# Kernel optimization log

Measured on AMD Instinct MI355X. Metric: run time of the kernel, lower is better.

The kernel has to match this reference:

```python
import jax, jax.numpy as jnp
import numpy as np

B, SEQ, DIM = 2, 4096, 1024
E, S = 8, 512          # num_slots = seq_len // num_experts
HID = 4 * DIM          # FeedForward hidden: dim * mult
SCALE = DIM ** 0.5     # RMSNorm scale


def rmsnorm(x, gamma):
    # matches F.normalize(x, dim=-1) * dim**0.5 * gamma (eps=1e-12 clamp on the norm)
    n = jnp.linalg.norm(x, axis=-1, keepdims=True)
    return x / jnp.maximum(n, 1e-12) * SCALE * gamma


def setup_inputs() -> dict:
    key = jax.random.key(0)
    ks = jax.random.split(key, 4)
    w_init = lambda k, shape: jax.random.normal(k, shape, dtype=jnp.float32) * 0.02
    return {
        "x": jax.random.normal(ks[0], (B, SEQ, DIM), dtype=jnp.float32),
        "norm_gamma": jnp.ones((DIM,), jnp.float32),
        "slot_norm_gamma": jnp.ones((DIM,), jnp.float32),
        "slot_embeds": jax.random.normal(ks[1], (E, S, DIM), dtype=jnp.float32),
        "w1": w_init(ks[2], (E, DIM, HID)),
        "b1": jnp.zeros((E, HID), jnp.float32),
        "w2": w_init(ks[3], (E, HID, DIM)),
        "b2": jnp.zeros((E, DIM), jnp.float32),
    }


def reference(x, norm_gamma, slot_norm_gamma, slot_embeds, w1, b1, w2, b2):
    xn = rmsnorm(x, norm_gamma)                 # [b, n, d]
    sn = rmsnorm(slot_embeds, slot_norm_gamma)  # [e, s, d]

    logits = jnp.einsum('bnd,esd->bnes', xn, sn)                   # [b, n, e, s]
    dispatch = jax.nn.softmax(logits, axis=1)                      # softmax over tokens n
    b, n, e, s = logits.shape
    combine = jax.nn.softmax(logits.reshape(b, n, e * s), axis=-1) # softmax over (e s)

    slots = jnp.einsum('bnd,bnes->besd', xn, dispatch)             # [b, e, s, d]

    # per-expert FeedForward: Linear -> GELU(exact) -> Linear (dropout=0)
    h = jnp.einsum('besd,edh->besh', slots, w1) + b1[None, :, None, :]
    h = jax.nn.gelu(h, approximate=False)
    eo = jnp.einsum('besh,ehd->besd', h, w2) + b2[None, :, None, :]

    eo = eo.reshape(b, e * s, DIM)                                 # [b, (e s), d]
    out = jnp.einsum('bmd,bnm->bnd', eo, combine)                  # [b, n, d]
    return out
```

## Files before the change

kernel.cpp:

```cpp
#include <hip/hip_runtime.h>
#include <math.h>

#define SEQ    4096
#define DIM    1024
#define NEXP   8
#define NSLOT  512
#define ES     4096
#define HID    4096
#define NB     2
#define RMS_SCALE 32.0f

typedef __attribute__((ext_vector_type(4))) float f32x4;
typedef __attribute__((ext_vector_type(8))) short bf16x8;
typedef __attribute__((ext_vector_type(4))) unsigned short us4;

__device__ __forceinline__ unsigned short f2bf(float f) {
    unsigned u = __float_as_uint(f);
    u += 0x7fff + ((u >> 16) & 1);
    return (unsigned short)(u >> 16);
}
__device__ __forceinline__ float bf2f(unsigned short h) {
    return __uint_as_float(((unsigned)h) << 16);
}
__device__ __forceinline__ float gelu_exact(float x) {
    return 0.5f * x * (1.0f + erff(x * 0.70710678118654752f));
}

#define GLOAD_LDS16(gp, lp) \
    __builtin_amdgcn_global_load_lds((const __attribute__((address_space(1))) void*)(gp), \
                                     (__attribute__((address_space(3))) void*)(lp), 16, 0, 0)

__device__ __forceinline__ unsigned ldsoff(const void* p) {
    return (unsigned)(size_t)(const __attribute__((address_space(3))) void*)p;
}

#define DSR(dst, base, off) asm volatile("ds_read_b128 %0, %1 offset:" off : "=v"(dst) : "v"(base))

template<int ORDER>
__global__ void rmsnorm_split(const float* __restrict__ in, const float* __restrict__ gamma,
                              unsigned short* __restrict__ outc) {
    int row = blockIdx.x;
    int t = threadIdx.x;
    float4 v = reinterpret_cast<const float4*>(in + (size_t)row * DIM)[t];
    float ss = v.x*v.x + v.y*v.y + v.z*v.z + v.w*v.w;
    #pragma unroll
    for (int off = 32; off >= 1; off >>= 1) ss += __shfl_down(ss, off, 64);
    __shared__ float red[4];
    if ((t & 63) == 0) red[t >> 6] = ss;
    __syncthreads();
    float inv = RMS_SCALE / fmaxf(sqrtf(red[0] + red[1] + red[2] + red[3]), 1e-12f);
    float4 g = reinterpret_cast<const float4*>(gamma)[t];
    float f[4] = {v.x*inv*g.x, v.y*inv*g.y, v.z*inv*g.z, v.w*inv*g.w};
    us4 hv, lv;
    #pragma unroll
    for (int q = 0; q < 4; ++q) {
        unsigned short h = f2bf(f[q]);
        hv[q] = h;
        lv[q] = f2bf(f[q] - bf2f(h));
    }
    unsigned short* rb = outc + (size_t)row * 3072;
    *reinterpret_cast<us4*>(&rb[t*4]) = hv;
    if (ORDER == 0) {
        *reinterpret_cast<us4*>(&rb[1024 + t*4]) = hv;
        *reinterpret_cast<us4*>(&rb[2048 + t*4]) = lv;
    } else {
        *reinterpret_cast<us4*>(&rb[1024 + t*4]) = lv;
        *reinterpret_cast<us4*>(&rb[2048 + t*4]) = hv;
    }
}

__global__ void col_stats_partial(const float* __restrict__ logits,
                                  float* __restrict__ pmax, float* __restrict__ psum) {
    int col = blockIdx.x * 256 + threadIdx.x;
    int ch  = blockIdx.y;
    int b   = blockIdx.z;
    const float* base = logits + ((size_t)b * SEQ + (size_t)ch * 512) * ES + col;
    float m = -INFINITY, s = 0.f;
    for (int n = 0; n < 512; ++n) {
        float v = base[(size_t)n * ES];
        float mn = fmaxf(m, v);
        s = s * __expf(m - mn) + __expf(v - mn);
        m = mn;
    }
    size_t idx = ((size_t)b * 8 + ch) * ES + col;
    pmax[idx] = m; psum[idx] = s;
}

__global__ void col_stats_reduce(const float* __restrict__ pmax, const float* __restrict__ psum,
                                 float* __restrict__ cmax, float* __restrict__ cinv) {
    int col = blockIdx.x * 256 + threadIdx.x;
    int b   = blockIdx.y;
    float m = -INFINITY, s = 0.f;
    for (int ch = 0; ch < 8; ++ch) {
        size_t idx = ((size_t)b * 8 + ch) * ES + col;
        float m2 = pmax[idx], s2 = psum[idx];
        float mn = fmaxf(m, m2);
        s = s * __expf(m - mn) + s2 * __expf(m2 - mn);
        m = mn;
    }
    cmax[(size_t)b * ES + col] = m;
    cinv[(size_t)b * ES + col] = 1.0f / s;
}

__global__ void row_stats(const float* __restrict__ logits,
                          float* __restrict__ rmax, float* __restrict__ rinv) {
    int row = blockIdx.x;
    int t = threadIdx.x;
    const float* base = logits + (size_t)row * ES;
    float m = -INFINITY, s = 0.f;
    for (int i = t; i < ES; i += 256) {
        float v = base[i];
        float mn = fmaxf(m, v);
        s = s * __expf(m - mn) + __expf(v - mn);
        m = mn;
    }
    __shared__ float sm[256], ssum[256];
    sm[t] = m; ssum[t] = s;
    __syncthreads();
    for (int off = 128; off >= 1; off >>= 1) {
        if (t < off) {
            float m1 = sm[t], m2 = sm[t+off], s1 = ssum[t], s2 = ssum[t+off];
            float mn = fmaxf(m1, m2);
            sm[t] = mn;
            ssum[t] = s1 * __expf(m1 - mn) + s2 * __expf(m2 - mn);
        }
        __syncthreads();
    }
    if (t == 0) { rmax[row] = sm[0]; rinv[row] = 1.0f / ssum[0]; }
}

__global__ void make_weights(const float* __restrict__ logits,
                             const float* __restrict__ cmax, const float* __restrict__ cinv,
                             const float* __restrict__ rmax, const float* __restrict__ rinv,
                             unsigned short* __restrict__ comb, unsigned short* __restrict__ dispT) {
    int b = blockIdx.z;
    const float* L = logits + (size_t)b * SEQ * ES;
    int n0 = blockIdx.y * 32, e0 = blockIdx.x * 32;
    int t = threadIdx.x;
    int r = t >> 3, c4 = (t & 7) * 4;
    __shared__ unsigned short tile[32][36];
    float4 v = *reinterpret_cast<const float4*>(&L[(size_t)(n0 + r) * ES + e0 + c4]);
    float rm = rmax[b*SEQ + n0 + r], ri = rinv[b*SEQ + n0 + r];
    float vv[4] = {v.x, v.y, v.z, v.w};
    us4 cb;
    #pragma unroll
    for (int q = 0; q < 4; ++q) {
        cb[q] = f2bf(__expf(vv[q] - rm) * ri);
        float dv = __expf(vv[q] - cmax[b*ES + e0 + c4 + q]) * cinv[b*ES + e0 + c4 + q];
        tile[c4 + q][r] = f2bf(dv);
    }
    *reinterpret_cast<us4*>(&comb[(size_t)b*SEQ*ES + (size_t)(n0 + r)*ES + e0 + c4]) = cb;
    __syncthreads();
    us4 o = *reinterpret_cast<us4*>(&tile[t >> 3][(t & 7) * 4]);
    *reinterpret_cast<us4*>(&dispT[(size_t)b*ES*SEQ + (size_t)(e0 + (t >> 3))*SEQ + n0 + (t & 7)*4]) = o;
}

__global__ void transpose_b16(const unsigned short* __restrict__ src, unsigned short* __restrict__ dst,
                              int sld, int dld, long sStride, long dStride) {
    int z = blockIdx.z;
    const unsigned short* S = src + (size_t)z * sStride;
    unsigned short* D = dst + (size_t)z * dStride;
    int r0 = blockIdx.y * 32, c0 = blockIdx.x * 32;
    int t = threadIdx.x;
    __shared__ unsigned short tile[32][36];
    us4 v = *reinterpret_cast<const us4*>(&S[(size_t)(r0 + (t>>3)) * sld + c0 + (t&7)*4]);
    #pragma unroll
    for (int q = 0; q < 4; ++q) tile[(t&7)*4 + q][t>>3] = v[q];
    __syncthreads();
    us4 o = *reinterpret_cast<us4*>(&tile[t >> 3][(t & 7) * 4]);
    *reinterpret_cast<us4*>(&D[(size_t)(c0 + (t>>3)) * dld + r0 + (t&7)*4]) = o;
}

__global__ void transpose_f32_b16(const float* __restrict__ src, unsigned short* __restrict__ dst,
                                  int sld, int dld, long sStride, long dStride) {
    int z = blockIdx.z;
    const float* S = src + (size_t)z * sStride;
    unsigned short* D = dst + (size_t)z * dStride;
    int r0 = blockIdx.y * 32, c0 = blockIdx.x * 32;
    int t = threadIdx.x;
    __shared__ unsigned short tile[32][36];
    float4 v = *reinterpret_cast<const float4*>(&S[(size_t)(r0 + (t>>3)) * sld + c0 + (t&7)*4]);
    float vv[4] = {v.x, v.y, v.z, v.w};
    #pragma unroll
    for (int q = 0; q < 4; ++q) tile[(t&7)*4 + q][t>>3] = f2bf(vv[q]);
    __syncthreads();
    us4 o = *reinterpret_cast<us4*>(&tile[t >> 3][(t & 7) * 4]);
    *reinterpret_cast<us4*>(&D[(size_t)(c0 + (t>>3)) * dld + r0 + (t&7)*4]) = o;
}

template<int EPI, int OM>
__global__ __launch_bounds__(512, 2)
void mfma_gemm256(const unsigned short* __restrict__ A, const unsigned short* __restrict__ B,
                  void* __restrict__ Cv, const float* __restrict__ bias,
                  int N, int K, int lda, int ldb, int ldc,
                  long aStride, long bStride, long cStride, int bMod) {
    __shared__ unsigned short lds[65536];
    const int t = threadIdx.x;
    const int lane = t & 63, wave = t >> 6;
    const int wr = wave >> 2, wc = wave & 3;
    const int z = blockIdx.z, zb = z % bMod;
    const unsigned short* Ab = A + (size_t)z * aStride;
    const unsigned short* Bb = B + (size_t)zb * bStride;
    const int gx = gridDim.x;
    int flat = blockIdx.x + blockIdx.y * gx;
    const int cpx = (gx * gridDim.y) >> 3;
    flat = (flat & 7) * cpx + (flat >> 3);
    const int m0 = (flat / gx) * 256, n0 = (flat % gx) * 256;

    const int sr = t >> 3;
    const int sg = (t & 7) ^ (sr & 7);
    const unsigned short* gA = Ab + (size_t)(m0 + sr) * lda + sg * 8;
    const unsigned short* gB = Bb + (size_t)(n0 + sr) * ldb + sg * 8;
    unsigned short* ldsw = lds + wave * 512;

    const int lr = lane & 15, lk = lane >> 4;
    const unsigned sw0 = (unsigned)(((lk)     ^ (lr & 7)) << 4);
    const unsigned sw1 = (unsigned)(((4 + lk) ^ (lr & 7)) << 4);
    const unsigned l0  = ldsoff(lds);
    const unsigned arow = (unsigned)((wr*128 + lr) * 128);
    const unsigned brow = (unsigned)((wc*64  + lr) * 128);
    const unsigned ab00 = l0 + arow + sw0,          ab10 = l0 + arow + sw1;
    const unsigned bb00 = l0 + 32768 + brow + sw0,  bb10 = l0 + 32768 + brow + sw1;
    const unsigned ab01 = ab00 + 65536, ab11 = ab10 + 65536;
    const unsigned bb01 = bb00 + 65536, bb11 = bb10 + 65536;

    #define STAGE_A(buf, half, tt) do { \
        const unsigned short* _g = gA + (size_t)((half)*128) * lda + (tt)*64; \
        unsigned short* _l = ldsw + (buf)*32768 + (half)*8192; \
        GLOAD_LDS16(_g, _l); \
        GLOAD_LDS16(_g + (size_t)64*lda, _l + 4096); } while(0)
    #define STAGE_B(buf, half, tt) do { \
        const unsigned short* _g = gB + (size_t)((half)*128) * ldb + (tt)*64; \
        unsigned short* _l = ldsw + (buf)*32768 + 16384 + (half)*8192; \
        GLOAD_LDS16(_g, _l); \
        GLOAD_LDS16(_g + (size_t)64*ldb, _l + 4096); } while(0)

    f32x4 acc[8][4] = {};
    bf16x8 a0[4], a1[4], b0[4], b1[4];

    const int NT = K / 64;

    STAGE_B(0, 0, 0); STAGE_B(0, 1, 0);
    STAGE_A(0, 0, 0); STAGE_A(0, 1, 0);
    STAGE_B(1, 0, 1); STAGE_B(1, 1, 1);
    asm volatile("s_waitcnt vmcnt(4)" ::: "memory");
    __builtin_amdgcn_s_barrier();

    #define PHASE_MFMA(MB, NB_) \
        __builtin_amdgcn_s_barrier(); \
        asm volatile("s_waitcnt lgkmcnt(0)" ::: "memory"); \
        __builtin_amdgcn_sched_barrier(0); \
        __builtin_amdgcn_s_setprio(1); \
        _Pragma("unroll") \
        for (int m = 0; m < 4; ++m) { \
            _Pragma("unroll") \
            for (int n = 0; n < 2; ++n) { \
                acc[MB+m][NB_+n] = __builtin_amdgcn_mfma_f32_16x16x32_bf16(a0[m], b0[NB_+n], acc[MB+m][NB_+n], 0, 0, 0); \
                acc[MB+m][NB_+n] = __builtin_amdgcn_mfma_f32_16x16x32_bf16(a1[m], b1[NB_+n], acc[MB+m][NB_+n], 0, 0, 0); \
            } \
        } \
        __builtin_amdgcn_s_setprio(0); \
        __builtin_amdgcn_sched_barrier(0); \
        __builtin_amdgcn_s_barrier();

    for (int tt = 0; tt < NT; tt += 2) {
        const bool pf = (tt + 2 < NT);
        DSR(a0[0], ab00, "0");    DSR(a0[1], ab00, "2048");
        DSR(a0[2], ab00, "4096"); DSR(a0[3], ab00, "6144");
        DSR(a1[0], ab10, "0");    DSR(a1[1], ab10, "2048");
        DSR(a1[2], ab10, "4096"); DSR(a1[3], ab10, "6144");
        DSR(b0[0], bb00, "0");    DSR(b0[1], bb00, "2048");
        DSR(b1[0], bb10, "0");    DSR(b1[1], bb10, "2048");
        STAGE_A(1, 0, tt+1);
        __builtin_amdgcn_sched_barrier(0);
        PHASE_MFMA(0, 0)
        DSR(b0[2], bb00, "4096"); DSR(b0[3], bb00, "6144");
        DSR(b1[2], bb10, "4096"); DSR(b1[3], bb10, "6144");
        STAGE_A(1, 1, tt+1);
        __builtin_amdgcn_sched_barrier(0);
        PHASE_MFMA(0, 2)
        DSR(a0[0], ab00, "8192");  DSR(a0[1], ab00, "10240");
        DSR(a0[2], ab00, "12288"); DSR(a0[3], ab00, "14336");
        DSR(a1[0], ab10, "8192");  DSR(a1[1], ab10, "10240");
        DSR(a1[2], ab10, "12288"); DSR(a1[3], ab10, "14336");
        if (pf) STAGE_B(0, 0, tt+2);
        __builtin_amdgcn_sched_barrier(0);
        PHASE_MFMA(4, 0)
        if (pf) STAGE_B(0, 1, tt+2);
        __builtin_amdgcn_sched_barrier(0);
        __builtin_amdgcn_s_barrier();
        __builtin_amdgcn_sched_barrier(0);
        __builtin_amdgcn_s_setprio(1);
        #pragma unroll
        for (int m = 0; m < 4; ++m) {
            #pragma unroll
            for (int n = 0; n < 2; ++n) {
                acc[4+m][2+n] = __builtin_amdgcn_mfma_f32_16x16x32_bf16(a0[m], b0[2+n], acc[4+m][2+n], 0, 0, 0);
                acc[4+m][2+n] = __builtin_amdgcn_mfma_f32_16x16x32_bf16(a1[m], b1[2+n], acc[4+m][2+n], 0, 0, 0);
            }
        }
        __builtin_amdgcn_s_setprio(0);
        if (pf) { asm volatile("s_waitcnt vmcnt(4)" ::: "memory"); }
        else    { asm volatile("s_waitcnt vmcnt(0)" ::: "memory"); }
        __builtin_amdgcn_sched_barrier(0);
        __builtin_amdgcn_s_barrier();
        DSR(a0[0], ab01, "0");    DSR(a0[1], ab01, "2048");
        DSR(a0[2], ab01, "4096"); DSR(a0[3], ab01, "6144");
        DSR(a1[0], ab11, "0");    DSR(a1[1], ab11, "2048");
        DSR(a1[2], ab11, "4096"); DSR(a1[3], ab11, "6144");
        DSR(b0[0], bb01, "0");    DSR(b0[1], bb01, "2048");
        DSR(b1[0], bb11, "0");    DSR(b1[1], bb11, "2048");
        if (pf) STAGE_A(0, 0, tt+2);
        __builtin_amdgcn_sched_barrier(0);
        PHASE_MFMA(0, 0)
        DSR(b0[2], bb01, "4096"); DSR(b0[3], bb01, "6144");
        DSR(b1[2], bb11, "4096"); DSR(b1[3], bb11, "6144");
        if (pf) STAGE_A(0, 1, tt+2);
        __builtin_amdgcn_sched_barrier(0);
        PHASE_MFMA(0, 2)
        DSR(a0[0], ab01, "8192");  DSR(a0[1], ab01, "10240");
        DSR(a0[2], ab01, "12288"); DSR(a0[3], ab01, "14336");
        DSR(a1[0], ab11, "8192");  DSR(a1[1], ab11, "10240");
        DSR(a1[2], ab11, "12288"); DSR(a1[3], ab11, "14336");
        if (pf) STAGE_B(1, 0, tt+3);
        __builtin_amdgcn_sched_barrier(0);
        PHASE_MFMA(4, 0)
        if (pf) STAGE_B(1, 1, tt+3);
        __builtin_amdgcn_sched_barrier(0);
        __builtin_amdgcn_s_barrier();
        __builtin_amdgcn_sched_barrier(0);
        __builtin_amdgcn_s_setprio(1);
        #pragma unroll
        for (int m = 0; m < 4; ++m) {
            #pragma unroll
            for (int n = 0; n < 2; ++n) {
                acc[4+m][2+n] = __builtin_amdgcn_mfma_f32_16x16x32_bf16(a0[m], b0[2+n], acc[4+m][2+n], 0, 0, 0);
                acc[4+m][2+n] = __builtin_amdgcn_mfma_f32_16x16x32_bf16(a1[m], b1[2+n], acc[4+m][2+n], 0, 0, 0);
            }
        }
        __builtin_amdgcn_s_setprio(0);
        if (pf) { asm volatile("s_waitcnt vmcnt(4)" ::: "memory"); }
        else    { asm volatile("s_waitcnt vmcnt(0)" ::: "memory"); }
        __builtin_amdgcn_sched_barrier(0);
        __builtin_amdgcn_s_barrier();
    }

    const float* bz = (EPI != 0) ? bias + (size_t)zb * N : nullptr;
    long coff = (long)z * cStride;
    int rbase = (lane >> 4) * 4;
    int cbase = lane & 15;
    #pragma unroll
    for (int f = 0; f < 8; ++f) {
        #pragma unroll
        for (int n = 0; n < 4; ++n) {
            int col  = n0 + wc*64 + n*16 + cbase;
            int row0 = m0 + wr*128 + f*16 + rbase;
            float bv = (EPI != 0) ? bz[col] : 0.f;
            float vals[4];
            #pragma unroll
            for (int r = 0; r < 4; ++r) {
                float v = acc[f][n][r] + bv;
                if (EPI == 2) v = gelu_exact(v);
                vals[r] = v;
            }
            if (OM == 0) {
                float* C = (float*)Cv + coff;
                #pragma unroll
                for (int r = 0; r < 4; ++r) C[(size_t)(row0 + r) * ldc + col] = vals[r];
            } else {
                unsigned short* C = (unsigned short*)Cv + coff;
                #pragma unroll
                for (int r = 0; r < 4; ++r) C[(size_t)(row0 + r) * ldc + col] = f2bf(vals[r]);
            }
        }
    }
    #undef STAGE_A
    #undef STAGE_B
    #undef PHASE_MFMA
}

template<int EPI, int OM>
__global__ __launch_bounds__(512, 2)
void mfma_gemmX(const unsigned short* __restrict__ A, const unsigned short* __restrict__ B,
                void* __restrict__ Cv, const float* __restrict__ bias,
                int N, int K, int lda, int ldb, int ldc,
                long aStride, long bStride, long cStride, long cStrideE, int bMod) {
    __shared__ unsigned short lds[49152];
    const int t = threadIdx.x;
    const int lane = t & 63, wave = t >> 6;
    const int wr = wave >> 2, wc = wave & 3;
    const int z = blockIdx.z, zb = z % bMod;
    const unsigned short* Ab = A + (size_t)z * aStride;
    const unsigned short* Bb = B + (size_t)zb * bStride;
    const int gx = gridDim.x;
    int flat = blockIdx.x + blockIdx.y * gx;
    const int cpx = (gx * gridDim.y) >> 3;
    flat = (flat & 7) * cpx + (flat >> 3);
    const int m0 = (flat / gx) * 256, n0 = (flat % gx) * 128;

    const int sr = t >> 3;
    const int sg = (t & 7) ^ (sr & 7);
    const unsigned short* gA = Ab + (size_t)(m0 + sr) * lda + sg * 8;
    const unsigned short* gB = Bb + (size_t)(n0 + sr) * ldb + sg * 8;
    unsigned short* ldsw = lds + wave * 512;

    const int lr = lane & 15, lk = lane >> 4;
    const unsigned g0 = (unsigned)(((lk)     ^ (lr & 7)) << 4);
    const unsigned g1 = (unsigned)(((4 + lk) ^ (lr & 7)) << 4);
    const unsigned l0 = ldsoff(lds);
    const unsigned arow = (unsigned)((wr*128 + lr) * 128);
    const unsigned brow = (unsigned)((wc*32  + lr) * 128);
    const unsigned axk0 = l0 + arow + g0,          axk1 = l0 + arow + g1;
    const unsigned bxk0 = l0 + 32768 + brow + g0,  bxk1 = l0 + 32768 + brow + g1;

    #define STAGE_AX(buf, half, tt) do { \
        const unsigned short* _g = gA + (size_t)((half)*128) * lda + (tt)*64; \
        unsigned short* _l = ldsw + (buf)*24576 + (half)*8192; \
        GLOAD_LDS16(_g, _l); \
        GLOAD_LDS16(_g + (size_t)64*lda, _l + 4096); } while(0)
    #define STAGE_BX(buf, tt) do { \
        const unsigned short* _g = gB + (tt)*64; \
        unsigned short* _l = ldsw + (buf)*24576 + 16384; \
        GLOAD_LDS16(_g, _l); \
        GLOAD_LDS16(_g + (size_t)64*ldb, _l + 4096); } while(0)

    f32x4 acc[8][2] = {};
    bf16x8 a0[4], a1[4], b0[2], b1[2];

    const int NT = K / 64;

    STAGE_BX(0, 0);
    STAGE_AX(0, 0, 0); STAGE_AX(0, 1, 0);
    STAGE_BX(1, 1);
    asm volatile("s_waitcnt vmcnt(2)" ::: "memory");
    __builtin_amdgcn_s_barrier();

    #define PHX(MB, AR, BR) \
        __builtin_amdgcn_s_barrier(); \
        asm volatile("s_waitcnt lgkmcnt(0)" ::: "memory"); \
        __builtin_amdgcn_sched_barrier(0); \
        __builtin_amdgcn_s_setprio(1); \
        _Pragma("unroll") \
        for (int m = 0; m < 4; ++m) { \
            _Pragma("unroll") \
            for (int n = 0; n < 2; ++n) { \
                acc[MB+m][n] = __builtin_amdgcn_mfma_f32_16x16x32_bf16(AR[m], BR[n], acc[MB+m][n], 0, 0, 0); \
            } \
        } \
        __builtin_amdgcn_s_setprio(0); \
        __builtin_amdgcn_sched_barrier(0); \
        __builtin_amdgcn_s_barrier();

    #define TILEX(AB0, AB1, BB0, BB1, SBUF, TT) { \
        const bool pf1 = (TT) + 1 < NT, pf2 = (TT) + 2 < NT; \
         \
        DSR(a0[0], AB0, "0");    DSR(a0[1], AB0, "2048"); \
        DSR(a0[2], AB0, "4096"); DSR(a0[3], AB0, "6144"); \
        DSR(b0[0], BB0, "0");    DSR(b0[1], BB0, "2048"); \
        if (pf1) STAGE_AX((SBUF)^1, 0, (TT)+1); \
        __builtin_amdgcn_sched_barrier(0); \
        PHX(0, a0, b0) \
         \
        DSR(a1[0], AB1, "0");    DSR(a1[1], AB1, "2048"); \
        DSR(a1[2], AB1, "4096"); DSR(a1[3], AB1, "6144"); \
        DSR(b1[0], BB1, "0");    DSR(b1[1], BB1, "2048"); \
        if (pf1) STAGE_AX((SBUF)^1, 1, (TT)+1); \
        __builtin_amdgcn_sched_barrier(0); \
        PHX(0, a1, b1) \
         \
        DSR(a0[0], AB0, "8192");  DSR(a0[1], AB0, "10240"); \
        DSR(a0[2], AB0, "12288"); DSR(a0[3], AB0, "14336"); \
        if (pf2) STAGE_BX(SBUF, (TT)+2); \
        __builtin_amdgcn_sched_barrier(0); \
        PHX(4, a0, b0) \
         \
        DSR(a1[0], AB1, "8192");  DSR(a1[1], AB1, "10240"); \
        DSR(a1[2], AB1, "12288"); DSR(a1[3], AB1, "14336"); \
        __builtin_amdgcn_sched_barrier(0); \
        __builtin_amdgcn_s_barrier(); \
        asm volatile("s_waitcnt lgkmcnt(0)" ::: "memory"); \
        __builtin_amdgcn_sched_barrier(0); \
        __builtin_amdgcn_s_setprio(1); \
        _Pragma("unroll") \
        for (int m = 0; m < 4; ++m) { \
            _Pragma("unroll") \
            for (int n = 0; n < 2; ++n) { \
                acc[4+m][n] = __builtin_amdgcn_mfma_f32_16x16x32_bf16(a1[m], b1[n], acc[4+m][n], 0, 0, 0); \
            } \
        } \
        __builtin_amdgcn_s_setprio(0); \
        if (pf2) { asm volatile("s_waitcnt vmcnt(2)" ::: "memory"); } \
        else     { asm volatile("s_waitcnt vmcnt(0)" ::: "memory"); } \
        __builtin_amdgcn_sched_barrier(0); \
        __builtin_amdgcn_s_barrier(); \
    }

    for (int tt = 0; tt < NT; tt += 2) {
        TILEX(axk0, axk1, bxk0, bxk1, 0, tt)
        TILEX(axk0 + 49152, axk1 + 49152, bxk0 + 49152, bxk1 + 49152, 1, tt + 1)
    }

    const float* bz = (EPI != 0) ? bias + (size_t)zb * N : nullptr;
    long coff = (long)z * cStride + (long)zb * cStrideE;
    int rbase = (lane >> 4) * 4;
    int cbase = lane & 15;
    #pragma unroll
    for (int f = 0; f < 8; ++f) {
        #pragma unroll
        for (int n = 0; n < 2; ++n) {
            int col  = n0 + wc*32 + n*16 + cbase;
            int row0 = m0 + wr*128 + f*16 + rbase;
            float bv = (EPI != 0) ? bz[col] : 0.f;
            float vals[4];
            #pragma unroll
            for (int r = 0; r < 4; ++r) {
                float v = acc[f][n][r] + bv;
                if (EPI == 2) v = gelu_exact(v);
                vals[r] = v;
            }
            if (OM == 0) {
                float* C = (float*)Cv + coff;
                #pragma unroll
                for (int r = 0; r < 4; ++r) C[(size_t)(row0 + r) * ldc + col] = vals[r];
            } else if (OM == 1) {
                unsigned short* C = (unsigned short*)Cv + coff;
                #pragma unroll
                for (int r = 0; r < 4; ++r) C[(size_t)(row0 + r) * ldc + col] = f2bf(vals[r]);
            } else {
                unsigned short* C = (unsigned short*)Cv + coff;
                us4 o;
                #pragma unroll
                for (int r = 0; r < 4; ++r) o[r] = f2bf(vals[r]);
                *reinterpret_cast<us4*>(&C[(size_t)col * ldc + row0]) = o;
            }
        }
    }
    #undef STAGE_AX
    #undef STAGE_BX
    #undef PHX
    #undef TILEX
}

extern "C" void kernel_launch(void* const* d_in, const int* in_sizes, int n_in,
                              void* d_out, int out_size, void* d_ws, size_t ws_size,
                              hipStream_t stream) {
    const float* x    = (const float*)d_in[0];
    const float* ng   = (const float*)d_in[1];
    const float* sg   = (const float*)d_in[2];
    const float* semb = (const float*)d_in[3];
    const float* w1   = (const float*)d_in[4];
    const float* b1   = (const float*)d_in[5];
    const float* w2   = (const float*)d_in[6];
    const float* b2   = (const float*)d_in[7];
    float* out = (float*)d_out;

    char* base = (char*)d_ws;
    unsigned short* Acat  = (unsigned short*)(base);
    unsigned short* Bcat  = (unsigned short*)(base + 50331648);
    unsigned short* dispT = (unsigned short*)(base);
    unsigned short* w2T   = (unsigned short*)(base);
    float*          logits= (float*)(base + 75497472);
    unsigned short* hbuf  = (unsigned short*)(base + 75497472);
    unsigned short* w1T   = (unsigned short*)(base + 142606336);
    unsigned short* xnT   = (unsigned short*)(base + 209715200);
    unsigned short* comb  = (unsigned short*)(base + 226492416);
    unsigned short* slots = (unsigned short*)(base + 293601280);
    unsigned short* eoT   = (unsigned short*)(base + 293601280);
    float* pmax = (float*)(base + 310378496);
    float* psum = pmax + 65536;
    float* cmax = psum + 65536;
    float* cinv = cmax + 8192;
    float* rmax = cinv + 8192;
    float* rinv = rmax + 8192;

    rmsnorm_split<0><<<NB*SEQ, 256, 0, stream>>>(x, ng, Acat);
    rmsnorm_split<1><<<NEXP*NSLOT, 256, 0, stream>>>(semb, sg, Bcat);

    transpose_b16<<<dim3(DIM/32, SEQ/32, NB), 256, 0, stream>>>(
        Acat, xnT, 3072, SEQ, (long)SEQ*3072, (long)DIM*SEQ);

    mfma_gemm256<0,0><<<dim3(ES/256, (NB*SEQ)/256, 1), 512, 0, stream>>>(
        Acat, Bcat, logits, nullptr, ES, 3072, 3072, 3072, ES,
        0L, 0L, 0L, 1);

    col_stats_partial<<<dim3(ES/256, 8, NB), 256, 0, stream>>>(logits, pmax, psum);
    col_stats_reduce<<<dim3(ES/256, NB), 256, 0, stream>>>(pmax, psum, cmax, cinv);
    row_stats<<<NB*SEQ, 256, 0, stream>>>(logits, rmax, rinv);

    make_weights<<<dim3(ES/32, SEQ/32, NB), 256, 0, stream>>>(
        logits, cmax, cinv, rmax, rinv, comb, dispT);

    transpose_f32_b16<<<dim3(HID/32, DIM/32, NEXP), 256, 0, stream>>>(
        w1, w1T, HID, DIM, (long)DIM*HID, (long)HID*DIM);

    mfma_gemmX<0,1><<<dim3(DIM/128, ES/256, NB), 512, 0, stream>>>(
        dispT, xnT, slots, nullptr, DIM, SEQ, SEQ, SEQ, DIM,
        (long)ES*SEQ, (long)DIM*SEQ, (long)ES*DIM, 0L, NB);

    transpose_f32_b16<<<dim3(DIM/32, HID/32, NEXP), 256, 0, stream>>>(
        w2, w2T, DIM, HID, (long)HID*DIM, (long)DIM*HID);

    mfma_gemm256<2,1><<<dim3(HID/256, NSLOT/256, NB*NEXP), 512, 0, stream>>>(
        slots, w1T, hbuf, b1, HID, DIM, DIM, DIM, HID,
        (long)NSLOT*DIM, (long)HID*DIM, (long)NSLOT*HID, NEXP);

    mfma_gemmX<1,2><<<dim3(DIM/128, NSLOT/256, NB*NEXP), 512, 0, stream>>>(
        hbuf, w2T, eoT, b2, DIM, HID, HID, HID, ES,
        (long)NSLOT*HID, (long)DIM*HID, (long)(DIM*ES/NEXP), (long)(NSLOT - DIM*ES/NEXP), NEXP);

    mfma_gemmX<0,0><<<dim3(DIM/128, SEQ/256, NB), 512, 0, stream>>>(
        comb, eoT, out, nullptr, DIM, ES, ES, ES, DIM,
        (long)SEQ*ES, (long)DIM*ES, (long)SEQ*DIM, 0L, NB);
}
```

Baseline: 720.1 us.

## Restructure GEMM LDS staging into quarter-tiles with finer-grained pipelined waits

Reorganizes how the 256x256 GEMM tiles are staged into LDS, splitting A and B loads into row quarters interleaved by 64/128 strides so each MFMA phase depends on a smaller slice of the prefetch. The waits are changed from a few coarse vmcnt points to per-phase vmcnt counts, which lets global-to-LDS loads for the next k-tiles overlap more of the MFMA work. The same restructuring is applied to both GEMM kernel variants. The tighter interleaving adds more barriers and depends on the vmcnt bookkeeping being exact, which risks stalls or races if the counts are wrong.

```diff
diff --git a/kernel.cpp b/kernel.cpp
--- a/kernel.cpp
+++ b/kernel.cpp
@@ -35,6 +35,13 @@
 }
 
 #define DSR(dst, base, off) asm volatile("ds_read_b128 %0, %1 offset:" off : "=v"(dst) : "v"(base))
+#define VM(n) asm volatile("s_waitcnt vmcnt(" #n ")" ::: "memory")
+#define BAR __builtin_amdgcn_s_barrier()
+#define SCB __builtin_amdgcn_sched_barrier(0)
+
+#define PH_OPEN  SCB; BAR; asm volatile("s_waitcnt lgkmcnt(0)" ::: "memory"); SCB; \
+                 __builtin_amdgcn_s_setprio(1);
+#define PH_CLOSE __builtin_amdgcn_s_setprio(0); SCB;
 
 template<int ORDER>
 __global__ void rmsnorm_split(const float* __restrict__ in, const float* __restrict__ gamma,
@@ -210,139 +217,106 @@
     const int sr = t >> 3;
     const int sg = (t & 7) ^ (sr & 7);
     const unsigned short* gA = Ab + (size_t)(m0 + sr) * lda + sg * 8;
-    const unsigned short* gB = Bb + (size_t)(n0 + sr) * ldb + sg * 8;
+    const int srB = sr + (sr & 32);
+    const unsigned short* gB = Bb + (size_t)(n0 + srB) * ldb + sg * 8;
     unsigned short* ldsw = lds + wave * 512;
 
     const int lr = lane & 15, lk = lane >> 4;
     const unsigned sw0 = (unsigned)(((lk)     ^ (lr & 7)) << 4);
     const unsigned sw1 = (unsigned)(((4 + lk) ^ (lr & 7)) << 4);
     const unsigned l0  = ldsoff(lds);
-    const unsigned arow = (unsigned)((wr*128 + lr) * 128);
-    const unsigned brow = (unsigned)((wc*64  + lr) * 128);
+    const unsigned arow = (unsigned)((wr*64 + lr) * 128);
+    const unsigned brow = (unsigned)((wc*32 + lr) * 128);
     const unsigned ab00 = l0 + arow + sw0,          ab10 = l0 + arow + sw1;
     const unsigned bb00 = l0 + 32768 + brow + sw0,  bb10 = l0 + 32768 + brow + sw1;
     const unsigned ab01 = ab00 + 65536, ab11 = ab10 + 65536;
     const unsigned bb01 = bb00 + 65536, bb11 = bb10 + 65536;
 
     #define STAGE_A(buf, half, tt) do { \
-        const unsigned short* _g = gA + (size_t)((half)*128) * lda + (tt)*64; \
+        const unsigned short* _g = gA + (size_t)((half)*64) * lda + (tt)*64; \
         unsigned short* _l = ldsw + (buf)*32768 + (half)*8192; \
         GLOAD_LDS16(_g, _l); \
-        GLOAD_LDS16(_g + (size_t)64*lda, _l + 4096); } while(0)
+        GLOAD_LDS16(_g + (size_t)128*lda, _l + 4096); } while(0)
     #define STAGE_B(buf, half, tt) do { \
-        const unsigned short* _g = gB + (size_t)((half)*128) * ldb + (tt)*64; \
+        const unsigned short* _g = gB + (size_t)((half)*32) * ldb + (tt)*64; \
         unsigned short* _l = ldsw + (buf)*32768 + 16384 + (half)*8192; \
         GLOAD_LDS16(_g, _l); \
-        GLOAD_LDS16(_g + (size_t)64*ldb, _l + 4096); } while(0)
-
-    f32x4 acc[8][4] = {};
-    bf16x8 a0[4], a1[4], b0[4], b1[4];
-
-    const int NT = K / 64;
-
-    STAGE_B(0, 0, 0); STAGE_B(0, 1, 0);
-    STAGE_A(0, 0, 0); STAGE_A(0, 1, 0);
-    STAGE_B(1, 0, 1); STAGE_B(1, 1, 1);
-    asm volatile("s_waitcnt vmcnt(4)" ::: "memory");
-    __builtin_amdgcn_s_barrier();
-
-    #define PHASE_MFMA(MB, NB_) \
-        __builtin_amdgcn_s_barrier(); \
-        asm volatile("s_waitcnt lgkmcnt(0)" ::: "memory"); \
-        __builtin_amdgcn_sched_barrier(0); \
-        __builtin_amdgcn_s_setprio(1); \
+        GLOAD_LDS16(_g + (size_t)128*ldb, _l + 4096); } while(0)
+
+    #define MFMA16(MB, CN) \
         _Pragma("unroll") \
         for (int m = 0; m < 4; ++m) { \
             _Pragma("unroll") \
             for (int n = 0; n < 2; ++n) { \
-                acc[MB+m][NB_+n] = __builtin_amdgcn_mfma_f32_16x16x32_bf16(a0[m], b0[NB_+n], acc[MB+m][NB_+n], 0, 0, 0); \
-                acc[MB+m][NB_+n] = __builtin_amdgcn_mfma_f32_16x16x32_bf16(a1[m], b1[NB_+n], acc[MB+m][NB_+n], 0, 0, 0); \
+                acc[(MB)+m][(CN)+n] = __builtin_amdgcn_mfma_f32_16x16x32_bf16(a0[m], b0[(CN)+n], acc[(MB)+m][(CN)+n], 0, 0, 0); \
+                acc[(MB)+m][(CN)+n] = __builtin_amdgcn_mfma_f32_16x16x32_bf16(a1[m], b1[(CN)+n], acc[(MB)+m][(CN)+n], 0, 0, 0); \
             } \
-        } \
-        __builtin_amdgcn_s_setprio(0); \
-        __builtin_amdgcn_sched_barrier(0); \
-        __builtin_amdgcn_s_barrier();
+        }
+
+    f32x4 acc[8][4] = {};
+    bf16x8 a0[4], a1[4], b0[4], b1[4];
+    const int NT = K / 64;
+
+    STAGE_A(0, 0, 0); STAGE_B(0, 0, 0); STAGE_B(0, 1, 0); STAGE_A(0, 1, 0);
+    STAGE_A(1, 0, 1); STAGE_B(1, 0, 1); STAGE_B(1, 1, 1);
+    VM(10); BAR;
 
     for (int tt = 0; tt < NT; tt += 2) {
-        const bool pf = (tt + 2 < NT);
+        const bool pf2 = (tt + 2 < NT);
+        const bool pf3 = (tt + 3 < NT);
         DSR(a0[0], ab00, "0");    DSR(a0[1], ab00, "2048");
         DSR(a0[2], ab00, "4096"); DSR(a0[3], ab00, "6144");
         DSR(a1[0], ab10, "0");    DSR(a1[1], ab10, "2048");
         DSR(a1[2], ab10, "4096"); DSR(a1[3], ab10, "6144");
         DSR(b0[0], bb00, "0");    DSR(b0[1], bb00, "2048");
         DSR(b1[0], bb10, "0");    DSR(b1[1], bb10, "2048");
-        STAGE_A(1, 0, tt+1);
-        __builtin_amdgcn_sched_barrier(0);
-        PHASE_MFMA(0, 0)
-        DSR(b0[2], bb00, "4096"); DSR(b0[3], bb00, "6144");
-        DSR(b1[2], bb10, "4096"); DSR(b1[3], bb10, "6144");
         STAGE_A(1, 1, tt+1);
-        __builtin_amdgcn_sched_barrier(0);
-        PHASE_MFMA(0, 2)
-        DSR(a0[0], ab00, "8192");  DSR(a0[1], ab00, "10240");
-        DSR(a0[2], ab00, "12288"); DSR(a0[3], ab00, "14336");
-        DSR(a1[0], ab10, "8192");  DSR(a1[1], ab10, "10240");
-        DSR(a1[2], ab10, "12288"); DSR(a1[3], ab10, "14336");
-        if (pf) STAGE_B(0, 0, tt+2);
-        __builtin_amdgcn_sched_barrier(0);
-        PHASE_MFMA(4, 0)
-        if (pf) STAGE_B(0, 1, tt+2);
-        __builtin_amdgcn_sched_barrier(0);
-        __builtin_amdgcn_s_barrier();
-        __builtin_amdgcn_sched_barrier(0);
-        __builtin_amdgcn_s_setprio(1);
-        #pragma unroll
-        for (int m = 0; m < 4; ++m) {
-            #pragma unroll
-            for (int n = 0; n < 2; ++n) {
-                acc[4+m][2+n] = __builtin_amdgcn_mfma_f32_16x16x32_bf16(a0[m], b0[2+n], acc[4+m][2+n], 0, 0, 0);
-                acc[4+m][2+n] = __builtin_amdgcn_mfma_f32_16x16x32_bf16(a1[m], b1[2+n], acc[4+m][2+n], 0, 0, 0);
-            }
-        }
-        __builtin_amdgcn_s_setprio(0);
-        if (pf) { asm volatile("s_waitcnt vmcnt(4)" ::: "memory"); }
-        else    { asm volatile("s_waitcnt vmcnt(0)" ::: "memory"); }
-        __builtin_amdgcn_sched_barrier(0);
-        __builtin_amdgcn_s_barrier();
+        PH_OPEN MFMA16(0, 0) PH_CLOSE
+        VM(10); BAR;
+        DSR(b0[2], bb00, "16384"); DSR(b0[3], bb00, "18432");
+        DSR(b1[2], bb10, "16384"); DSR(b1[3], bb10, "18432");
+        if (pf2) STAGE_A(0, 0, tt+2);
+        PH_OPEN MFMA16(0, 2) PH_CLOSE
+        if (pf2) { VM(10); } else { VM(8); }
+        BAR;
+        DSR(a0[0], ab00, "16384"); DSR(a0[1], ab00, "18432");
+        DSR(a0[2], ab00, "20480"); DSR(a0[3], ab00, "22528");
+        DSR(a1[0], ab10, "16384"); DSR(a1[1], ab10, "18432");
+        DSR(a1[2], ab10, "20480"); DSR(a1[3], ab10, "22528");
+        if (pf2) STAGE_B(0, 0, tt+2);
+        PH_OPEN MFMA16(4, 0) PH_CLOSE
+        BAR;
+        if (pf2) STAGE_B(0, 1, tt+2);
+        PH_OPEN MFMA16(4, 2) PH_CLOSE
+        if (pf2) { VM(10); } else { VM(4); }
+        BAR;
         DSR(a0[0], ab01, "0");    DSR(a0[1], ab01, "2048");
         DSR(a0[2], ab01, "4096"); DSR(a0[3], ab01, "6144");
         DSR(a1[0], ab11, "0");    DSR(a1[1], ab11, "2048");
         DSR(a1[2], ab11, "4096"); DSR(a1[3], ab11, "6144");
         DSR(b0[0], bb01, "0");    DSR(b0[1], bb01, "2048");
         DSR(b1[0], bb11, "0");    DSR(b1[1], bb11, "2048");
-        if (pf) STAGE_A(0, 0, tt+2);
-        __builtin_amdgcn_sched_barrier(0);
-        PHASE_MFMA(0, 0)
-        DSR(b0[2], bb01, "4096"); DSR(b0[3], bb01, "6144");
-        DSR(b1[2], bb11, "4096"); DSR(b1[3], bb11, "6144");
-        if (pf) STAGE_A(0, 1, tt+2);
-        __builtin_amdgcn_sched_barrier(0);
-        PHASE_MFMA(0, 2)
-        DSR(a0[0], ab01, "8192");  DSR(a0[1], ab01, "10240");
-        DSR(a0[2], ab01, "12288"); DSR(a0[3], ab01, "14336");
-        DSR(a1[0], ab11, "8192");  DSR(a1[1], ab11, "10240");
-        DSR(a1[2], ab11, "12288"); DSR(a1[3], ab11, "14336");
-        if (pf) STAGE_B(1, 0, tt+3);
-        __builtin_amdgcn_sched_barrier(0);
-        PHASE_MFMA(4, 0)
-        if (pf) STAGE_B(1, 1, tt+3);
-        __builtin_amdgcn_sched_barrier(0);
-        __builtin_amdgcn_s_barrier();
-        __builtin_amdgcn_sched_barrier(0);
-        __builtin_amdgcn_s_setprio(1);
-        #pragma unroll
-        for (int m = 0; m < 4; ++m) {
-            #pragma unroll
-            for (int n = 0; n < 2; ++n) {
-                acc[4+m][2+n] = __builtin_amdgcn_mfma_f32_16x16x32_bf16(a0[m], b0[2+n], acc[4+m][2+n], 0, 0, 0);
-                acc[4+m][2+n] = __builtin_amdgcn_mfma_f32_16x16x32_bf16(a1[m], b1[2+n], acc[4+m][2+n], 0, 0, 0);
-            }
-        }
-        __builtin_amdgcn_s_setprio(0);
-        if (pf) { asm volatile("s_waitcnt vmcnt(4)" ::: "memory"); }
-        else    { asm volatile("s_waitcnt vmcnt(0)" ::: "memory"); }
-        __builtin_amdgcn_sched_barrier(0);
-        __builtin_amdgcn_s_barrier();
+        if (pf2) STAGE_A(0, 1, tt+2);
+        PH_OPEN MFMA16(0, 0) PH_CLOSE
+        if (pf2) { VM(10); } else { VM(2); }
+        BAR;
+        DSR(b0[2], bb01, "16384"); DSR(b0[3], bb01, "18432");
+        DSR(b1[2], bb11, "16384"); DSR(b1[3], bb11, "18432");
+        if (pf3) STAGE_A(1, 0, tt+3);
+        PH_OPEN MFMA16(0, 2) PH_CLOSE
+        if (pf2) { VM(10); } else { VM(0); }
+        BAR;
+        DSR(a0[0], ab01, "16384"); DSR(a0[1], ab01, "18432");
+        DSR(a0[2], ab01, "20480"); DSR(a0[3], ab01, "22528");
+        DSR(a1[0], ab11, "16384"); DSR(a1[1], ab11, "18432");
+        DSR(a1[2], ab11, "20480"); DSR(a1[3], ab11, "22528");
+        if (pf3) STAGE_B(1, 0, tt+3);
+        PH_OPEN MFMA16(4, 0) PH_CLOSE
+        BAR;
+        if (pf3) STAGE_B(1, 1, tt+3);
+        PH_OPEN MFMA16(4, 2) PH_CLOSE
+        if (pf2) { VM(10); } else { VM(0); }
+        BAR;
     }
 
     const float* bz = (EPI != 0) ? bias + (size_t)zb * N : nullptr;
@@ -376,7 +350,7 @@
     }
     #undef STAGE_A
     #undef STAGE_B
-    #undef PHASE_MFMA
+    #undef MFMA16
 }
 
 template<int EPI, int OM>
@@ -408,96 +382,89 @@
     const unsigned g0 = (unsigned)(((lk)     ^ (lr & 7)) << 4);
     const unsigned g1 = (unsigned)(((4 + lk) ^ (lr & 7)) << 4);
     const unsigned l0 = ldsoff(lds);
-    const unsigned arow = (unsigned)((wr*128 + lr) * 128);
-    const unsigned brow = (unsigned)((wc*32  + lr) * 128);
-    const unsigned axk0 = l0 + arow + g0,          axk1 = l0 + arow + g1;
-    const unsigned bxk0 = l0 + 32768 + brow + g0,  bxk1 = l0 + 32768 + brow + g1;
-
-    #define STAGE_AX(buf, half, tt) do { \
-        const unsigned short* _g = gA + (size_t)((half)*128) * lda + (tt)*64; \
-        unsigned short* _l = ldsw + (buf)*24576 + (half)*8192; \
+    const unsigned arow = (unsigned)((wr*64 + lr) * 128);
+    const unsigned brow = (unsigned)((wc*32 + lr) * 128);
+    const unsigned ax00 = l0 + arow + g0,          ax10 = l0 + arow + g1;
+    const unsigned bx00 = l0 + 32768 + brow + g0,  bx10 = l0 + 32768 + brow + g1;
+    const unsigned ax01 = ax00 + 49152, ax11 = ax10 + 49152;
+    const unsigned bx01 = bx00 + 49152, bx11 = bx10 + 49152;
+
+    #define STAGE_AX(buf, quad, tt) do { \
+        const unsigned short* _g = gA + (size_t)((quad)*64) * lda + (tt)*64; \
+        unsigned short* _l = ldsw + (buf)*24576 + (quad)*8192; \
         GLOAD_LDS16(_g, _l); \
-        GLOAD_LDS16(_g + (size_t)64*lda, _l + 4096); } while(0)
+        GLOAD_LDS16(_g + (size_t)128*lda, _l + 4096); } while(0)
     #define STAGE_BX(buf, tt) do { \
         const unsigned short* _g = gB + (tt)*64; \
         unsigned short* _l = ldsw + (buf)*24576 + 16384; \
         GLOAD_LDS16(_g, _l); \
         GLOAD_LDS16(_g + (size_t)64*ldb, _l + 4096); } while(0)
 
-    f32x4 acc[8][2] = {};
-    bf16x8 a0[4], a1[4], b0[2], b1[2];
-
-    const int NT = K / 64;
-
-    STAGE_BX(0, 0);
-    STAGE_AX(0, 0, 0); STAGE_AX(0, 1, 0);
-    STAGE_BX(1, 1);
-    asm volatile("s_waitcnt vmcnt(2)" ::: "memory");
-    __builtin_amdgcn_s_barrier();
-
-    #define PHX(MB, AR, BR) \
-        __builtin_amdgcn_s_barrier(); \
-        asm volatile("s_waitcnt lgkmcnt(0)" ::: "memory"); \
-        __builtin_amdgcn_sched_barrier(0); \
-        __builtin_amdgcn_s_setprio(1); \
+    #define MFMA8(MB, AR, BR) \
         _Pragma("unroll") \
         for (int m = 0; m < 4; ++m) { \
             _Pragma("unroll") \
             for (int n = 0; n < 2; ++n) { \
-                acc[MB+m][n] = __builtin_amdgcn_mfma_f32_16x16x32_bf16(AR[m], BR[n], acc[MB+m][n], 0, 0, 0); \
+                acc[(MB)+m][n] = __builtin_amdgcn_mfma_f32_16x16x32_bf16(AR[m], BR[n], acc[(MB)+m][n], 0, 0, 0); \
             } \
-        } \
-        __builtin_amdgcn_s_setprio(0); \
-        __builtin_amdgcn_sched_barrier(0); \
-        __builtin_amdgcn_s_barrier();
-
-    #define TILEX(AB0, AB1, BB0, BB1, SBUF, TT) { \
-        const bool pf1 = (TT) + 1 < NT, pf2 = (TT) + 2 < NT; \
-         \
-        DSR(a0[0], AB0, "0");    DSR(a0[1], AB0, "2048"); \
-        DSR(a0[2], AB0, "4096"); DSR(a0[3], AB0, "6144"); \
-        DSR(b0[0], BB0, "0");    DSR(b0[1], BB0, "2048"); \
-        if (pf1) STAGE_AX((SBUF)^1, 0, (TT)+1); \
-        __builtin_amdgcn_sched_barrier(0); \
-        PHX(0, a0, b0) \
-         \
-        DSR(a1[0], AB1, "0");    DSR(a1[1], AB1, "2048"); \
-        DSR(a1[2], AB1, "4096"); DSR(a1[3], AB1, "6144"); \
-        DSR(b1[0], BB1, "0");    DSR(b1[1], BB1, "2048"); \
-        if (pf1) STAGE_AX((SBUF)^1, 1, (TT)+1); \
-        __builtin_amdgcn_sched_barrier(0); \
-        PHX(0, a1, b1) \
-         \
-        DSR(a0[0], AB0, "8192");  DSR(a0[1], AB0, "10240"); \
-        DSR(a0[2], AB0, "12288"); DSR(a0[3], AB0, "14336"); \
-        if (pf2) STAGE_BX(SBUF, (TT)+2); \
-        __builtin_amdgcn_sched_barrier(0); \
-        PHX(4, a0, b0) \
-         \
-        DSR(a1[0], AB1, "8192");  DSR(a1[1], AB1, "10240"); \
-        DSR(a1[2], AB1, "12288"); DSR(a1[3], AB1, "14336"); \
-        __builtin_amdgcn_sched_barrier(0); \
-        __builtin_amdgcn_s_barrier(); \
-        asm volatile("s_waitcnt lgkmcnt(0)" ::: "memory"); \
-        __builtin_amdgcn_sched_barrier(0); \
-        __builtin_amdgcn_s_setprio(1); \
-        _Pragma("unroll") \
-        for (int m = 0; m < 4; ++m) { \
-            _Pragma("unroll") \
-            for (int n = 0; n < 2; ++n) { \
-                acc[4+m][n] = __builtin_amdgcn_mfma_f32_16x16x32_bf16(a1[m], b1[n], acc[4+m][n], 0, 0, 0); \
-            } \
-        } \
-        __builtin_amdgcn_s_setprio(0); \
-        if (pf2) { asm volatile("s_waitcnt vmcnt(2)" ::: "memory"); } \
-        else     { asm volatile("s_waitcnt vmcnt(0)" ::: "memory"); } \
-        __builtin_amdgcn_sched_barrier(0); \
-        __builtin_amdgcn_s_barrier(); \
-    }
+        }
+
+    f32x4 acc[8][2] = {};
+    bf16x8 a0[4], a1[4], b0[2], b1[2];
+    const int NT = K / 64;
+
+    STAGE_AX(0, 0, 0); STAGE_BX(0, 0); STAGE_AX(0, 1, 0);
+    STAGE_AX(1, 0, 1); STAGE_BX(1, 1);
+    VM(6); BAR;
 
     for (int tt = 0; tt < NT; tt += 2) {
-        TILEX(axk0, axk1, bxk0, bxk1, 0, tt)
-        TILEX(axk0 + 49152, axk1 + 49152, bxk0 + 49152, bxk1 + 49152, 1, tt + 1)
+        const bool pf2 = (tt + 2 < NT);
+        const bool pf3 = (tt + 3 < NT);
+        DSR(a0[0], ax00, "0");    DSR(a0[1], ax00, "2048");
+        DSR(a0[2], ax00, "4096"); DSR(a0[3], ax00, "6144");
+        DSR(b0[0], bx00, "0");    DSR(b0[1], bx00, "2048");
+        STAGE_AX(1, 1, tt+1);
+        PH_OPEN MFMA8(0, a0, b0) PH_CLOSE
+        BAR;
+        DSR(a1[0], ax10, "0");    DSR(a1[1], ax10, "2048");
+        DSR(a1[2], ax10, "4096"); DSR(a1[3], ax10, "6144");
+        DSR(b1[0], bx10, "0");    DSR(b1[1], bx10, "2048");
+        PH_OPEN MFMA8(0, a1, b1) PH_CLOSE
+        VM(6); BAR;
+        DSR(a0[0], ax00, "16384"); DSR(a0[1], ax00, "18432");
+        DSR(a0[2], ax00, "20480"); DSR(a0[3], ax00, "22528");
+        if (pf2) STAGE_AX(0, 0, tt+2);
+        PH_OPEN MFMA8(4, a0, b0) PH_CLOSE
+        BAR;
+        DSR(a1[0], ax10, "16384"); DSR(a1[1], ax10, "18432");
+        DSR(a1[2], ax10, "20480"); DSR(a1[3], ax10, "22528");
+        if (pf2) STAGE_BX(0, tt+2);
+        PH_OPEN MFMA8(4, a1, b1) PH_CLOSE
+        if (pf2) { VM(6); } else { VM(2); }
+        BAR;
+        DSR(a0[0], ax01, "0");    DSR(a0[1], ax01, "2048");
+        DSR(a0[2], ax01, "4096"); DSR(a0[3], ax01, "6144");
+        DSR(b0[0], bx01, "0");    DSR(b0[1], bx01, "2048");
+        if (pf2) STAGE_AX(0, 1, tt+2);
+        PH_OPEN MFMA8(0, a0, b0) PH_CLOSE
+        BAR;
+        DSR(a1[0], ax11, "0");    DSR(a1[1], ax11, "2048");
+        DSR(a1[2], ax11, "4096"); DSR(a1[3], ax11, "6144");
+        DSR(b1[0], bx11, "0");    DSR(b1[1], bx11, "2048");
+        PH_OPEN MFMA8(0, a1, b1) PH_CLOSE
+        if (pf2) { VM(6); } else { VM(0); }
+        BAR;
+        DSR(a0[0], ax01, "16384"); DSR(a0[1], ax01, "18432");
+        DSR(a0[2], ax01, "20480"); DSR(a0[3], ax01, "22528");
+        if (pf3) STAGE_AX(1, 0, tt+3);
+        PH_OPEN MFMA8(4, a0, b0) PH_CLOSE
+        BAR;
+        DSR(a1[0], ax11, "16384"); DSR(a1[1], ax11, "18432");
+        DSR(a1[2], ax11, "20480"); DSR(a1[3], ax11, "22528");
+        if (pf3) STAGE_BX(1, tt+3);
+        PH_OPEN MFMA8(4, a1, b1) PH_CLOSE
+        if (pf2) { VM(6); } else { VM(0); }
+        BAR;
     }
 
     const float* bz = (EPI != 0) ? bias + (size_t)zb * N : nullptr;
@@ -537,8 +504,7 @@
     }
     #undef STAGE_AX
     #undef STAGE_BX
-    #undef PHX
-    #undef TILEX
+    #undef MFMA8
 }
 
 extern "C" void kernel_launch(void* const* d_in, const int* in_sizes, int n_in,
```

After: 707.9 us. Within noise of the previous version (-1.7%).
